# Performance work log

Measured on AMD Instinct MI355X. Metric: run time of the kernel, lower is better.

## Reference

```python
import jax, jax.numpy as jnp
import numpy as np

STEPS = 8

def wn_linear(x, v, g, b):
    # PyTorch weight_norm (dim=0): w = g * v / ||v||_row
    w = v * (g / jnp.linalg.norm(v, axis=1, keepdims=True))
    return x @ w.T + b

def setup_inputs() -> dict:
    key = jax.random.key(0)
    ks = jax.random.split(key, 24)
    N, L, H = 65536, 256, 512
    D = L + 3
    inp = {
        'input': jax.random.normal(ks[0], (N, D), jnp.float32),
        # LSTMCell params
        'W_ih': jax.random.normal(ks[1], (4 * H, D), jnp.float32) * (1.0 / np.sqrt(D)),
        'b_ih': jnp.zeros((4 * H,), jnp.float32),
        'W_hh': jax.random.normal(ks[2], (4 * H, H), jnp.float32) * (1.0 / np.sqrt(H)),
        'b_hh': jnp.zeros((4 * H,), jnp.float32).at[H:2 * H].set(1.0),  # forget-gate init
        # affine out layer (initialized tiny in the original)
        'W_aff': jax.random.normal(ks[3], (6, H), jnp.float32) * 1e-3,
        'b_aff': jnp.zeros((6,), jnp.float32),
    }
    # SdfDecoder: lin0..lin4 weight-normed, lin5 plain
    dims_in = [3, 256, 256, 256, 256]
    for i, din in enumerate(dims_in):
        inp[f'v{i}'] = jax.random.normal(ks[4 + 2 * i], (256, din), jnp.float32) * (1.0 / np.sqrt(din))
        inp[f'g{i}'] = jnp.linalg.norm(inp[f'v{i}'], axis=1, keepdims=True)
        inp[f'b{i}'] = jnp.zeros((256,), jnp.float32)
    inp['W5'] = jax.random.normal(ks[20], (1, 256), jnp.float32) * (1.0 / 16.0)
    inp['b5'] = jnp.zeros((1,), jnp.float32)
    return inp

def warp(code, xyz0, W_ih, b_ih, W_hh, b_hh, W_aff, b_aff):
    N = code.shape[0]
    H = W_hh.shape[1]
    def step(carry, _):
        h, c, xyz = carry
        x = jnp.concatenate([code, xyz], axis=1)               # [N, L+3]
        gates = x @ W_ih.T + b_ih + h @ W_hh.T + b_hh          # [N, 4H]
        i, f, g, o = jnp.split(gates, 4, axis=1)
        c = jax.nn.sigmoid(f) * c + jax.nn.sigmoid(i) * jnp.tanh(g)
        h = o_ = jax.nn.sigmoid(o) * jnp.tanh(c)
        a = h @ W_aff.T + b_aff                                # [N, 6]
        xyz = a[:, 3:] + (1.0 + a[:, :3]) * xyz                # addcmul
        return (h, c, xyz), None
    z = jnp.zeros((N, H), code.dtype)
    (_, _, xyz), _ = jax.lax.scan(step, (z, z, xyz0), None, length=STEPS)
    return xyz

def sdf_decoder(p, v0, g0, b0, v1, g1, b1, v2, g2, b2, v3, g3, b3, v4, g4, b4, W5, b5):
    x = jax.nn.relu(wn_linear(p, v0, g0, b0))   # eval mode: dropout is identity
    x = jax.nn.relu(wn_linear(x, v1, g1, b1))
    x = jax.nn.relu(wn_linear(x, v2, g2, b2))
    x = jax.nn.relu(wn_linear(x, v3, g3, b3))
    x = jax.nn.relu(wn_linear(x, v4, g4, b4))
    return x @ W5.T + b5

def reference(input, W_ih, b_ih, W_hh, b_hh, W_aff, b_aff,
              v0, g0, b0, v1, g1, b1, v2, g2, b2, v3, g3, b3, v4, g4, b4, W5, b5):
    code, xyz = input[:, :-3], input[:, -3:]
    p_final = warp(code, xyz, W_ih, b_ih, W_hh, b_hh, W_aff, b_aff)
    return sdf_decoder(p_final, v0, g0, b0, v1, g1, b1, v2, g2, b2, v3, g3, b3, v4, g4, b4, W5, b5)
```

## Files before the change

kernel.cpp:

```cpp
#include <hip/hip_runtime.h>
#include <stdint.h>


typedef short v8s __attribute__((ext_vector_type(8)));
typedef float v4f __attribute__((ext_vector_type(4)));

#define MFMA16(a, b, c) __builtin_amdgcn_mfma_f32_16x16x32_bf16((a), (b), (c), 0, 0, 0)

static __device__ __forceinline__ unsigned short f2bf(float f) {
  union { float f; uint32_t u; } x; x.f = f;
  uint32_t u = x.u;
  return (unsigned short)((u + 0x7fffu + ((u >> 16) & 1u)) >> 16);
}
static __device__ __forceinline__ float bf2f(unsigned short s) {
  union { uint32_t u; float f; } x; x.u = ((uint32_t)s) << 16; return x.f;
}
static __device__ __forceinline__ float sigf(float x) {
  return 1.f / (1.f + __expf(-x));
}
static __device__ __forceinline__ float tanh_fast(float x) {
  float e = __expf(2.f * x);
  return 1.f - 2.f / (e + 1.f);
}

static __device__ __forceinline__ void gload16(const void* g, void* l) {
  __builtin_amdgcn_global_load_lds(
      (const __attribute__((address_space(1))) uint32_t*)g,
      (__attribute__((address_space(3))) uint32_t*)l, 16, 0, 0);
}

#define WS_LSTMPK 0
#define WS_LSTMPK_ELEMS 1638400
#define WS_AFFPK 3276800
#define WS_AFFPK_ELEMS 8192
#define WS_DECPK 3293184
#define WS_DECPK_ELEMS 262144
#define WS_DSCALE 3817472
#define WS_TOTAL 3821568

#define OFF_H     0
#define OFF_RING  65536
#define OFF_AFF   114688
#define OFF_BIASP 131072
#define OFF_XYZ   139264
#define OFF_A     140288
#define OFF_W0N   142336
#define OFF_B0    145408
#define OFF_DB    146432
#define OFF_W5    150528
#define OFF_MISC  151552
#define SMEM_BYTES 151616

__global__ void dec_norm_kernel(const float* __restrict__ v1, const float* __restrict__ v2,
                                const float* __restrict__ v3, const float* __restrict__ v4,
                                const float* __restrict__ g1, const float* __restrict__ g2,
                                const float* __restrict__ g3, const float* __restrict__ g4,
                                float* __restrict__ dscale) {
  int L = blockIdx.x;
  int row = threadIdx.x;
  const float* v = (L == 0) ? v1 : (L == 1) ? v2 : (L == 2) ? v3 : v4;
  const float* g = (L == 0) ? g1 : (L == 1) ? g2 : (L == 2) ? g3 : g4;
  float s = 0.f;
  for (int k = 0; k < 256; ++k) { float x = v[row * 256 + k]; s += x * x; }
  dscale[L * 256 + row] = g[row] / sqrtf(s);
}

__global__ void pack_kernel(const float* __restrict__ W_ih, const float* __restrict__ W_hh,
                            const float* __restrict__ W_aff,
                            const float* __restrict__ v1, const float* __restrict__ v2,
                            const float* __restrict__ v3, const float* __restrict__ v4,
                            const float* __restrict__ dscale,
                            unsigned short* __restrict__ lstmpk,
                            unsigned short* __restrict__ affpk,
                            unsigned short* __restrict__ decpk) {
  int i = blockIdx.x * 256 + threadIdx.x;
  if (i < WS_LSTMPK_ELEMS) {
    int j = i & 7; int rest = i >> 3;
    int l = rest & 63; rest >>= 6;
    int fi = rest & 15; rest >>= 4;
    int tb = rest % 25; int c = rest / 25;
    int kl = 8 * (l >> 4) + j;
    int grow = (fi & 3) * 512 + c * 64 + (fi >> 2) * 16 + (l & 15);
    float val;
    if (tb < 8)       val = W_ih[(size_t)grow * 259 + tb * 32 + kl];
    else if (tb == 8) val = (kl < 3) ? W_ih[(size_t)grow * 259 + 256 + kl] : 0.f;
    else              val = W_hh[(size_t)grow * 512 + (tb - 9) * 32 + kl];
    lstmpk[i] = f2bf(val);
  } else if (i < WS_LSTMPK_ELEMS + WS_AFFPK_ELEMS) {
    int ii = i - WS_LSTMPK_ELEMS;
    int j = ii & 7, l = (ii >> 3) & 63, t = ii >> 9;
    int k = 32 * t + 8 * (l >> 4) + j;
    int col = l & 15;
    float val = (col < 6) ? W_aff[col * 512 + k] : 0.f;
    affpk[ii] = f2bf(val);
  } else {
    int ii = i - (WS_LSTMPK_ELEMS + WS_AFFPK_ELEMS);
    int j = ii & 7, l = (ii >> 3) & 63, fi = (ii >> 9) & 15, t = (ii >> 13) & 7, L = ii >> 16;
    int k = 32 * t + 8 * (l >> 4) + j;
    int col = 16 * fi + (l & 15);
    const float* v = (L == 0) ? v1 : (L == 1) ? v2 : (L == 2) ? v3 : v4;
    float val = v[col * 256 + k] * dscale[L * 256 + col];
    decpk[ii] = f2bf(val);
  }
}

__global__ __launch_bounds__(512, 1) void lstm_main(
    const float* __restrict__ input,
    const float* __restrict__ b_ih, const float* __restrict__ b_hh,
    const float* __restrict__ b_aff,
    const float* __restrict__ v0, const float* __restrict__ g0, const float* __restrict__ b0,
    const float* __restrict__ b1, const float* __restrict__ b2,
    const float* __restrict__ b3, const float* __restrict__ b4,
    const float* __restrict__ W5, const float* __restrict__ b5,
    const unsigned short* __restrict__ lstmpk,
    const unsigned short* __restrict__ affpk,
    const unsigned short* __restrict__ decpk,
    float* __restrict__ out) {
  extern __shared__ char smem[];
  float* smf = (float*)smem;

  const int tid = threadIdx.x;
  const int lane = tid & 63;
  const int wid = tid >> 6;
  const int l15 = lane & 15;
  const int lg = lane >> 4;
  const int rowg = wid & 1;
  const int colq = wid >> 1;
  const int r0 = blockIdx.x * 64;

  const int arow0 = rowg * 32 + l15;
  const int arow1 = arow0 + 16;
  const uint32_t a_sw = (uint32_t)((l15 & 7) << 4);
  const uint32_t hbase0 = OFF_H + (uint32_t)arow0 * 1024;
  const uint32_t hbase1 = OFF_H + (uint32_t)arow1 * 1024;
  const char* lstm_c = (const char*)lstmpk;
  const char* dec_c = (const char*)decpk;

  {
    uint4 z = make_uint4(0, 0, 0, 0);
    for (int i = tid; i < 4096; i += 512) *(uint4*)(smem + OFF_H + (size_t)i * 16) = z;
  }
  if (tid < 192) {
    int row = tid / 3, d = tid - row * 3;
    smf[OFF_XYZ / 4 + row * 4 + d] = input[(size_t)(r0 + row) * 259 + 256 + d];
  }
  for (int i = tid; i < 2048; i += 512) {
    int c = i >> 8, jc = i & 255, n = jc >> 4, t15 = jc & 15;
    int grow = (n & 3) * 512 + c * 64 + (n >> 2) * 16 + t15;
    smf[OFF_BIASP / 4 + i] = b_ih[grow] + b_hh[grow];
  }
  if (tid < 256) {
    int u = tid;
    float a0 = v0[u * 3 + 0], a1 = v0[u * 3 + 1], a2 = v0[u * 3 + 2];
    float sc = g0[u] / sqrtf(a0 * a0 + a1 * a1 + a2 * a2);
    smf[OFF_W0N / 4 + u * 3 + 0] = a0 * sc;
    smf[OFF_W0N / 4 + u * 3 + 1] = a1 * sc;
    smf[OFF_W0N / 4 + u * 3 + 2] = a2 * sc;
    smf[OFF_B0 / 4 + u] = b0[u];
    smf[OFF_DB / 4 + 0 * 256 + u] = b1[u];
    smf[OFF_DB / 4 + 1 * 256 + u] = b2[u];
    smf[OFF_DB / 4 + 2 * 256 + u] = b3[u];
    smf[OFF_DB / 4 + 3 * 256 + u] = b4[u];
    smf[OFF_W5 / 4 + u] = W5[u];
  }
  if (tid < 6) smf[OFF_MISC / 4 + tid] = b_aff[tid];
  if (tid == 6) smf[OFF_MISC / 4 + 6] = b5[0];
  {
    const char* src = (const char*)affpk + (((size_t)(2 * wid)) << 10) + (size_t)lane * 16;
    char* dst = smem + OFF_AFF + ((2 * wid) << 10);
    gload16(src, dst);
    gload16(src + 1024, dst + 1024);
  }

  v8s codeA0[8], codeA1[8];
  {
    const float* cr0 = input + (size_t)(r0 + arow0) * 259;
    const float* cr1 = input + (size_t)(r0 + arow1) * 259;
#pragma unroll
    for (int t = 0; t < 8; ++t) {
      v8s a0v = {0, 0, 0, 0, 0, 0, 0, 0}, a1v = {0, 0, 0, 0, 0, 0, 0, 0};
#pragma unroll
      for (int j = 0; j < 8; ++j) {
        a0v[j] = (short)f2bf(cr0[t * 32 + lg * 8 + j]);
        a1v[j] = (short)f2bf(cr1[t * 32 + lg * 8 + j]);
      }
      codeA0[t] = a0v; codeA1[t] = a1v;
    }
  }
  __syncthreads();

  float creg[8][8];
#pragma unroll
  for (int c = 0; c < 8; ++c)
#pragma unroll
    for (int e = 0; e < 8; ++e) creg[c][e] = 0.f;
  uint32_t hst[8][4];

  for (int step = 0; step < 8; ++step) {
    v8s xyzA0 = {0, 0, 0, 0, 0, 0, 0, 0}, xyzA1 = {0, 0, 0, 0, 0, 0, 0, 0};
    if (lg == 0) {
      xyzA0[0] = (short)f2bf(smf[OFF_XYZ / 4 + arow0 * 4 + 0]);
      xyzA0[1] = (short)f2bf(smf[OFF_XYZ / 4 + arow0 * 4 + 1]);
      xyzA0[2] = (short)f2bf(smf[OFF_XYZ / 4 + arow0 * 4 + 2]);
      xyzA1[0] = (short)f2bf(smf[OFF_XYZ / 4 + arow1 * 4 + 0]);
      xyzA1[1] = (short)f2bf(smf[OFF_XYZ / 4 + arow1 * 4 + 1]);
      xyzA1[2] = (short)f2bf(smf[OFF_XYZ / 4 + arow1 * 4 + 2]);
    }

    int cs = 0, tbs = 0, rs = 2, sb = 0;
    {
      const char* s0 = lstm_c + (((size_t)(2 * wid)) << 10) + (size_t)lane * 16;
      char* d0 = smem + OFF_RING + ((2 * wid) << 10);
      gload16(s0, d0); gload16(s0 + 1024, d0 + 1024);
      const char* s1 = lstm_c + (((size_t)(16 + 2 * wid)) << 10) + (size_t)lane * 16;
      char* d1 = smem + OFF_RING + 16384 + ((2 * wid) << 10);
      gload16(s1, d1); gload16(s1 + 1024, d1 + 1024);
      tbs = 2;
    }

#pragma unroll
    for (int c = 0; c < 8; ++c) {
      v4f acc0[4], acc1[4];
#pragma unroll
      for (int fi = 0; fi < 4; ++fi) {
        float bb = smf[OFF_BIASP / 4 + c * 256 + (colq * 4 + fi) * 16 + l15];
        acc0[fi][0] = bb; acc0[fi][1] = bb; acc0[fi][2] = bb; acc0[fi][3] = bb;
        acc1[fi][0] = bb; acc1[fi][1] = bb; acc1[fi][2] = bb; acc1[fi][3] = bb;
      }

      auto phase = [&](v8s af0, v8s af1, bool last) {
        if (last) { asm volatile("s_waitcnt vmcnt(0)" ::: "memory"); }
        else      { asm volatile("s_waitcnt vmcnt(2)" ::: "memory"); }
        __builtin_amdgcn_s_barrier();
        if (cs < 8) {
          const char* src = lstm_c + (((size_t)((cs * 25 + tbs) * 16 + 2 * wid)) << 10)
                          + (size_t)lane * 16;
          char* dst = smem + OFF_RING + rs * 16384 + ((2 * wid) << 10);
          gload16(src, dst);
          gload16(src + 1024, dst + 1024);
          rs = (rs == 2) ? 0 : rs + 1;
          if (++tbs == 25) { tbs = 0; ++cs; }
        }
        const char* sl = smem + OFF_RING + sb * 16384 + (colq << 12) + (lane << 4);
        __builtin_amdgcn_s_setprio(1);
#pragma unroll
        for (int fi = 0; fi < 4; ++fi) {
          v8s bf = *(const v8s*)(sl + (fi << 10));
          acc0[fi] = MFMA16(af0, bf, acc0[fi]);
          acc1[fi] = MFMA16(af1, bf, acc1[fi]);
        }
        __builtin_amdgcn_s_setprio(0);
        sb = (sb == 2) ? 0 : sb + 1;
      };

#pragma unroll
      for (int t = 0; t < 8; ++t) phase(codeA0[t], codeA1[t], false);
      phase(xyzA0, xyzA1, false);
#pragma unroll 2
      for (int t2 = 0; t2 < 16; ++t2) {
        uint32_t ko = (uint32_t)(t2 * 32 + lg * 8) * 2;
        v8s af0 = *(const v8s*)(smem + hbase0 + (ko ^ a_sw));
        v8s af1 = *(const v8s*)(smem + hbase1 + (ko ^ a_sw));
        phase(af0, af1, (c == 7) && (t2 == 15));
      }

#define CELLUP(AQ, M) do {                                                   \
        uint32_t plo = 0, phi = 0;                                           \
        _Pragma("unroll")                                                    \
        for (int j = 0; j < 4; ++j) {                                        \
          float gi = AQ[0][j], gf = AQ[1][j], gg = AQ[2][j], go = AQ[3][j];  \
          float cc = creg[c][(M) * 4 + j];                                   \
          cc = sigf(gf) * cc + sigf(gi) * tanh_fast(gg);                     \
          creg[c][(M) * 4 + j] = cc;                                         \
          uint32_t hb = f2bf(sigf(go) * tanh_fast(cc));                      \
          if (j < 2) plo |= hb << (16 * j); else phi |= hb << (16 * (j - 2));\
        }                                                                    \
        hst[c][(M) * 2 + 0] = plo; hst[c][(M) * 2 + 1] = phi; } while (0)
      CELLUP(acc0, 0);
      CELLUP(acc1, 1);
#undef CELLUP
    }

    __syncthreads();
#pragma unroll
    for (int c = 0; c < 8; ++c)
#pragma unroll
      for (int m = 0; m < 2; ++m)
#pragma unroll
        for (int j = 0; j < 4; ++j) {
          int u = c * 64 + colq * 16 + l15;
          int rr = rowg * 32 + m * 16 + lg * 4 + j;
          uint32_t val = ((j < 2) ? (hst[c][m * 2] >> (16 * j))
                                  : (hst[c][m * 2 + 1] >> (16 * (j - 2)))) & 0xffffu;
          *(unsigned short*)(smem + OFF_H + (uint32_t)rr * 1024 +
                             (uint32_t)((u * 2) ^ ((rr & 7) << 4))) = (unsigned short)val;
        }
    __syncthreads();
    if (wid < 2) {
      v4f a0 = {0.f, 0.f, 0.f, 0.f}, a1v = {0.f, 0.f, 0.f, 0.f};
#pragma unroll 2
      for (int t = 0; t < 16; ++t) {
        uint32_t ko = (uint32_t)(t * 32 + lg * 8) * 2;
        v8s bf = *(const v8s*)(smem + OFF_AFF + (t << 10) + (lane << 4));
        v8s af0 = *(const v8s*)(smem + hbase0 + (ko ^ a_sw));
        v8s af1 = *(const v8s*)(smem + hbase1 + (ko ^ a_sw));
        a0 = MFMA16(af0, bf, a0);
        a1v = MFMA16(af1, bf, a1v);
      }
      if (l15 < 6) {
        float ba = smf[OFF_MISC / 4 + l15];
#pragma unroll
        for (int j = 0; j < 4; ++j) {
          smf[OFF_A / 4 + (rowg * 32 + lg * 4 + j) * 8 + l15] = a0[j] + ba;
          smf[OFF_A / 4 + (rowg * 32 + 16 + lg * 4 + j) * 8 + l15] = a1v[j] + ba;
        }
      }
    }
    __syncthreads();
    if (tid < 192) {
      int rr = tid / 3, d = tid - rr * 3;
      float ad = smf[OFF_A / 4 + rr * 8 + d];
      float a3 = smf[OFF_A / 4 + rr * 8 + 3 + d];
      float old = smf[OFF_XYZ / 4 + rr * 4 + d];
      smf[OFF_XYZ / 4 + rr * 4 + d] = a3 + (1.f + ad) * old;
    }
    __syncthreads();
  }

  {
    const char* s0 = dec_c + (((size_t)(2 * wid)) << 10) + (size_t)lane * 16;
    char* d0 = smem + OFF_RING + ((2 * wid) << 10);
    gload16(s0, d0); gload16(s0 + 1024, d0 + 1024);
    const char* s1 = dec_c + (((size_t)(16 + 2 * wid)) << 10) + (size_t)lane * 16;
    char* d1 = smem + OFF_RING + 16384 + ((2 * wid) << 10);
    gload16(s1, d1); gload16(s1 + 1024, d1 + 1024);
  }
  {
    int row = tid & 63;
    int ublk = tid >> 6;
    float p0 = smf[OFF_XYZ / 4 + row * 4 + 0];
    float p1 = smf[OFF_XYZ / 4 + row * 4 + 1];
    float p2 = smf[OFF_XYZ / 4 + row * 4 + 2];
#pragma unroll
    for (int gq = 0; gq < 4; ++gq) {
      int u0 = ublk * 32 + gq * 8;
      uint32_t pk[4];
#pragma unroll
      for (int jj = 0; jj < 8; ++jj) {
        int uu = u0 + jj;
        float val = smf[OFF_B0 / 4 + uu]
                  + smf[OFF_W0N / 4 + uu * 3 + 0] * p0
                  + smf[OFF_W0N / 4 + uu * 3 + 1] * p1
                  + smf[OFF_W0N / 4 + uu * 3 + 2] * p2;
        val = fmaxf(val, 0.f);
        ((unsigned short*)pk)[jj] = f2bf(val);
      }
      *(uint4*)(smem + OFF_H + (uint32_t)row * 512 +
                (uint32_t)((u0 * 2) ^ ((row & 7) << 4))) = *(uint4*)pk;
    }
  }
  __syncthreads();

  {
    int ps = 2, rs = 2, sb = 0;
#pragma unroll
    for (int L = 0; L < 4; ++L) {
      v4f acc0[4], acc1[4];
#pragma unroll
      for (int fi = 0; fi < 4; ++fi) {
        float bb = smf[OFF_DB / 4 + L * 256 + (colq * 4 + fi) * 16 + l15];
        acc0[fi][0] = bb; acc0[fi][1] = bb; acc0[fi][2] = bb; acc0[fi][3] = bb;
        acc1[fi][0] = bb; acc1[fi][1] = bb; acc1[fi][2] = bb; acc1[fi][3] = bb;
      }
      uint32_t xin = OFF_H + (uint32_t)((L & 1) * 32768);
      uint32_t ab0 = xin + (uint32_t)arow0 * 512;
      uint32_t ab1 = xin + (uint32_t)arow1 * 512;
#pragma unroll
      for (int t = 0; t < 8; ++t) {
        uint32_t ko = (uint32_t)(t * 32 + lg * 8) * 2;
        v8s af0 = *(const v8s*)(smem + ab0 + (ko ^ a_sw));
        v8s af1 = *(const v8s*)(smem + ab1 + (ko ^ a_sw));
        if (L == 3 && t == 7) { asm volatile("s_waitcnt vmcnt(0)" ::: "memory"); }
        else                  { asm volatile("s_waitcnt vmcnt(2)" ::: "memory"); }
        __builtin_amdgcn_s_barrier();
        if (ps < 32) {
          const char* src = dec_c + (((size_t)(ps * 16 + 2 * wid)) << 10) + (size_t)lane * 16;
          char* dst = smem + OFF_RING + rs * 16384 + ((2 * wid) << 10);
          gload16(src, dst);
          gload16(src + 1024, dst + 1024);
          ps++;
          rs = (rs == 2) ? 0 : rs + 1;
        }
        const char* sl = smem + OFF_RING + sb * 16384 + (colq << 12) + (lane << 4);
        __builtin_amdgcn_s_setprio(1);
#pragma unroll
        for (int fi = 0; fi < 4; ++fi) {
          v8s bf = *(const v8s*)(sl + (fi << 10));
          acc0[fi] = MFMA16(af0, bf, acc0[fi]);
          acc1[fi] = MFMA16(af1, bf, acc1[fi]);
        }
        __builtin_amdgcn_s_setprio(0);
        sb = (sb == 2) ? 0 : sb + 1;
      }
      uint32_t xout = OFF_H + (uint32_t)(((L + 1) & 1) * 32768);
#pragma unroll
      for (int fi = 0; fi < 4; ++fi) {
        int coli = (colq * 4 + fi) * 16 + l15;
#pragma unroll
        for (int j = 0; j < 4; ++j) {
          int rr0 = rowg * 32 + lg * 4 + j;
          int rr1 = rr0 + 16;
          *(unsigned short*)(smem + xout + (uint32_t)rr0 * 512 +
                             (uint32_t)((coli * 2) ^ ((rr0 & 7) << 4))) = f2bf(fmaxf(acc0[fi][j], 0.f));
          *(unsigned short*)(smem + xout + (uint32_t)rr1 * 512 +
                             (uint32_t)((coli * 2) ^ ((rr1 & 7) << 4))) = f2bf(fmaxf(acc1[fi][j], 0.f));
        }
      }
      __syncthreads();
    }
  }

  {
    float b5v = smf[OFF_MISC / 4 + 6];
    for (int rr = 0; rr < 8; ++rr) {
      int r = wid * 8 + rr;
      uint32_t byteoff = OFF_H + (uint32_t)r * 512 + (uint32_t)((lane * 8) ^ ((r & 7) << 4));
      uint2 xv = *(const uint2*)(smem + byteoff);
      float p = 0.f;
#pragma unroll
      for (int jj = 0; jj < 4; ++jj) {
        unsigned short us = (unsigned short)(((jj < 2) ? (xv.x >> (16 * jj))
                                                       : (xv.y >> (16 * (jj - 2)))) & 0xffffu);
        p += bf2f(us) * smf[OFF_W5 / 4 + lane * 4 + jj];
      }
#pragma unroll
      for (int off = 32; off >= 1; off >>= 1) p += __shfl_xor(p, off, 64);
      if (lane == 0) out[r0 + r] = p + b5v;
    }
  }
}

extern "C" void kernel_launch(void* const* d_in, const int* in_sizes, int n_in,
                              void* d_out, int out_size, void* d_ws, size_t ws_size,
                              hipStream_t stream) {
  const float* input = (const float*)d_in[0];
  const float* W_ih  = (const float*)d_in[1];
  const float* b_ih  = (const float*)d_in[2];
  const float* W_hh  = (const float*)d_in[3];
  const float* b_hh  = (const float*)d_in[4];
  const float* W_aff = (const float*)d_in[5];
  const float* b_aff = (const float*)d_in[6];
  const float* v0 = (const float*)d_in[7];
  const float* g0 = (const float*)d_in[8];
  const float* b0 = (const float*)d_in[9];
  const float* v1 = (const float*)d_in[10];
  const float* g1 = (const float*)d_in[11];
  const float* b1 = (const float*)d_in[12];
  const float* v2 = (const float*)d_in[13];
  const float* g2 = (const float*)d_in[14];
  const float* b2 = (const float*)d_in[15];
  const float* v3 = (const float*)d_in[16];
  const float* g3 = (const float*)d_in[17];
  const float* b3 = (const float*)d_in[18];
  const float* v4 = (const float*)d_in[19];
  const float* g4 = (const float*)d_in[20];
  const float* b4 = (const float*)d_in[21];
  const float* W5 = (const float*)d_in[22];
  const float* b5 = (const float*)d_in[23];

  char* ws = (char*)d_ws;
  unsigned short* lstmpk = (unsigned short*)(ws + WS_LSTMPK);
  unsigned short* affpk  = (unsigned short*)(ws + WS_AFFPK);
  unsigned short* decpk  = (unsigned short*)(ws + WS_DECPK);
  float* dscale = (float*)(ws + WS_DSCALE);
  float* outp = (float*)d_out;

  (void)in_sizes; (void)n_in; (void)out_size; (void)ws_size;

  hipFuncSetAttribute((const void*)lstm_main,
                      hipFuncAttributeMaxDynamicSharedMemorySize, SMEM_BYTES);

  dec_norm_kernel<<<4, 256, 0, stream>>>(v1, v2, v3, v4, g1, g2, g3, g4, dscale);
  pack_kernel<<<7456, 256, 0, stream>>>(W_ih, W_hh, W_aff, v1, v2, v3, v4, dscale,
                                        lstmpk, affpk, decpk);
  lstm_main<<<1024, 512, SMEM_BYTES, stream>>>(
      input, b_ih, b_hh, b_aff, v0, g0, b0, b1, b2, b3, b4, W5, b5,
      lstmpk, affpk, decpk, outp);
}
```

Baseline: 4.223 ms.

## Skip zero-state recurrent GEMM, stage code in LDS, rotate weight chunk order

At step 0 the recurrent h·W_hh phases are skipped, because h starts at zero. The bf16 code operand moves from per-thread registers into a swizzled LDS buffer, which frees VGPRs. The affine weights now stream through the shared ring buffer as a final slab, and the next step's first slabs are prefetched during the xyz update. Each block also rotates which gate chunk it starts on, to spread L2 traffic, and several biases and the first-layer weights are stored as bf16 in LDS. That last change loses a little precision.

```diff
diff --git a/kernel.cpp b/kernel.cpp
--- a/kernel.cpp
+++ b/kernel.cpp
@@ -40,16 +40,16 @@
 
 #define OFF_H     0
 #define OFF_RING  65536
-#define OFF_AFF   114688
-#define OFF_BIASP 131072
-#define OFF_XYZ   139264
-#define OFF_A     140288
-#define OFF_W0N   142336
-#define OFF_B0    145408
-#define OFF_DB    146432
-#define OFF_W5    150528
-#define OFF_MISC  151552
-#define SMEM_BYTES 151616
+#define OFF_CODE  114688
+#define OFF_BIASP 147456
+#define OFF_XYZ   151552
+#define OFF_A     152576
+#define OFF_W0N   154624
+#define OFF_B0    156160
+#define OFF_DB    157184
+#define OFF_W5    159232
+#define OFF_MISC  160256
+#define SMEM_BYTES 160288
 
 __global__ void dec_norm_kernel(const float* __restrict__ v1, const float* __restrict__ v2,
                                 const float* __restrict__ v3, const float* __restrict__ v4,
@@ -118,6 +118,7 @@
     float* __restrict__ out) {
   extern __shared__ char smem[];
   float* smf = (float*)smem;
+  uint16_t* smh = (uint16_t*)smem;
 
   const int tid = threadIdx.x;
   const int lane = tid & 63;
@@ -127,18 +128,44 @@
   const int rowg = wid & 1;
   const int colq = wid >> 1;
   const int r0 = blockIdx.x * 64;
+  const int rot = blockIdx.x & 7;
 
   const int arow0 = rowg * 32 + l15;
   const int arow1 = arow0 + 16;
   const uint32_t a_sw = (uint32_t)((l15 & 7) << 4);
   const uint32_t hbase0 = OFF_H + (uint32_t)arow0 * 1024;
   const uint32_t hbase1 = OFF_H + (uint32_t)arow1 * 1024;
+  const uint32_t cbase0 = OFF_CODE + (uint32_t)arow0 * 512;
+  const uint32_t cbase1 = OFF_CODE + (uint32_t)arow1 * 512;
   const char* lstm_c = (const char*)lstmpk;
+  const char* aff_c = (const char*)affpk;
   const char* dec_c = (const char*)decpk;
 
+  auto stage_slab = [&](const char* slab_base, int slot) {
+    const char* src = slab_base + ((2 * wid) << 10) + (size_t)lane * 16;
+    char* dst = smem + OFF_RING + slot * 16384 + ((2 * wid) << 10);
+    gload16(src, dst);
+    gload16(src + 1024, dst + 1024);
+  };
+
   {
-    uint4 z = make_uint4(0, 0, 0, 0);
-    for (int i = tid; i < 4096; i += 512) *(uint4*)(smem + OFF_H + (size_t)i * 16) = z;
+    int row = tid >> 3;
+    int kb0 = (tid & 7) * 8;
+    const float* src0 = input + (size_t)(r0 + row) * 259;
+#pragma unroll
+    for (int it = 0; it < 4; ++it) {
+      int kb = kb0 + it * 64;
+      const float* src = src0 + kb;
+      uint32_t p[4];
+#pragma unroll
+      for (int jj = 0; jj < 4; ++jj) {
+        float f0 = src[2 * jj], f1 = src[2 * jj + 1];
+        p[jj] = (uint32_t)f2bf(f0) | ((uint32_t)f2bf(f1) << 16);
+      }
+      uint32_t byteoff = OFF_CODE + (uint32_t)row * 512 +
+                         (uint32_t)((kb * 2) ^ ((row & 7) << 4));
+      *(uint4*)(smem + byteoff) = make_uint4(p[0], p[1], p[2], p[3]);
+    }
   }
   if (tid < 192) {
     int row = tid / 3, d = tid - row * 3;
@@ -147,47 +174,28 @@
   for (int i = tid; i < 2048; i += 512) {
     int c = i >> 8, jc = i & 255, n = jc >> 4, t15 = jc & 15;
     int grow = (n & 3) * 512 + c * 64 + (n >> 2) * 16 + t15;
-    smf[OFF_BIASP / 4 + i] = b_ih[grow] + b_hh[grow];
+    smh[OFF_BIASP / 2 + i] = f2bf(b_ih[grow] + b_hh[grow]);
   }
   if (tid < 256) {
     int u = tid;
     float a0 = v0[u * 3 + 0], a1 = v0[u * 3 + 1], a2 = v0[u * 3 + 2];
     float sc = g0[u] / sqrtf(a0 * a0 + a1 * a1 + a2 * a2);
-    smf[OFF_W0N / 4 + u * 3 + 0] = a0 * sc;
-    smf[OFF_W0N / 4 + u * 3 + 1] = a1 * sc;
-    smf[OFF_W0N / 4 + u * 3 + 2] = a2 * sc;
+    smh[OFF_W0N / 2 + u * 3 + 0] = f2bf(a0 * sc);
+    smh[OFF_W0N / 2 + u * 3 + 1] = f2bf(a1 * sc);
+    smh[OFF_W0N / 2 + u * 3 + 2] = f2bf(a2 * sc);
     smf[OFF_B0 / 4 + u] = b0[u];
-    smf[OFF_DB / 4 + 0 * 256 + u] = b1[u];
-    smf[OFF_DB / 4 + 1 * 256 + u] = b2[u];
-    smf[OFF_DB / 4 + 2 * 256 + u] = b3[u];
-    smf[OFF_DB / 4 + 3 * 256 + u] = b4[u];
+    smh[OFF_DB / 2 + 0 * 256 + u] = f2bf(b1[u]);
+    smh[OFF_DB / 2 + 1 * 256 + u] = f2bf(b2[u]);
+    smh[OFF_DB / 2 + 2 * 256 + u] = f2bf(b3[u]);
+    smh[OFF_DB / 2 + 3 * 256 + u] = f2bf(b4[u]);
     smf[OFF_W5 / 4 + u] = W5[u];
   }
   if (tid < 6) smf[OFF_MISC / 4 + tid] = b_aff[tid];
   if (tid == 6) smf[OFF_MISC / 4 + 6] = b5[0];
-  {
-    const char* src = (const char*)affpk + (((size_t)(2 * wid)) << 10) + (size_t)lane * 16;
-    char* dst = smem + OFF_AFF + ((2 * wid) << 10);
-    gload16(src, dst);
-    gload16(src + 1024, dst + 1024);
-  }
-
-  v8s codeA0[8], codeA1[8];
-  {
-    const float* cr0 = input + (size_t)(r0 + arow0) * 259;
-    const float* cr1 = input + (size_t)(r0 + arow1) * 259;
-#pragma unroll
-    for (int t = 0; t < 8; ++t) {
-      v8s a0v = {0, 0, 0, 0, 0, 0, 0, 0}, a1v = {0, 0, 0, 0, 0, 0, 0, 0};
-#pragma unroll
-      for (int j = 0; j < 8; ++j) {
-        a0v[j] = (short)f2bf(cr0[t * 32 + lg * 8 + j]);
-        a1v[j] = (short)f2bf(cr1[t * 32 + lg * 8 + j]);
-      }
-      codeA0[t] = a0v; codeA1[t] = a1v;
-    }
-  }
   __syncthreads();
+
+  stage_slab(lstm_c + ((size_t)(rot * 25) << 14), 0);
+  stage_slab(lstm_c + ((size_t)(rot * 25 + 1) << 14), 1);
 
   float creg[8][8];
 #pragma unroll
@@ -197,6 +205,9 @@
   uint32_t hst[8][4];
 
   for (int step = 0; step < 8; ++step) {
+    const int per_c = step ? 25 : 9;
+    const int count = per_c * 8 + 1;
+
     v8s xyzA0 = {0, 0, 0, 0, 0, 0, 0, 0}, xyzA1 = {0, 0, 0, 0, 0, 0, 0, 0};
     if (lg == 0) {
       xyzA0[0] = (short)f2bf(smf[OFF_XYZ / 4 + arow0 * 4 + 0]);
@@ -207,116 +218,129 @@
       xyzA1[2] = (short)f2bf(smf[OFF_XYZ / 4 + arow1 * 4 + 2]);
     }
 
-    int cs = 0, tbs = 0, rs = 2, sb = 0;
-    {
-      const char* s0 = lstm_c + (((size_t)(2 * wid)) << 10) + (size_t)lane * 16;
-      char* d0 = smem + OFF_RING + ((2 * wid) << 10);
-      gload16(s0, d0); gload16(s0 + 1024, d0 + 1024);
-      const char* s1 = lstm_c + (((size_t)(16 + 2 * wid)) << 10) + (size_t)lane * 16;
-      char* d1 = smem + OFF_RING + 16384 + ((2 * wid) << 10);
-      gload16(s1, d1); gload16(s1 + 1024, d1 + 1024);
-      tbs = 2;
-    }
-
-#pragma unroll
-    for (int c = 0; c < 8; ++c) {
-      v4f acc0[4], acc1[4];
+    int sS = 2, stbs = 2, scs_phys = rot, rs = 2, sb = 0;
+
+    v4f acc0[4], acc1[4];
+    auto phz = [&](v8s af0, v8s af1) {
+      asm volatile("s_waitcnt vmcnt(2)" ::: "memory");
+      __builtin_amdgcn_s_barrier();
+      if (sS < count) {
+        const char* src;
+        if (sS == count - 1) {
+          src = aff_c + ((2 * wid) << 10) + (size_t)lane * 16;
+        } else {
+          src = lstm_c + (((size_t)((scs_phys * 25 + stbs) * 16 + 2 * wid)) << 10)
+              + (size_t)lane * 16;
+          if (++stbs == per_c) { stbs = 0; scs_phys = (scs_phys + 1) & 7; }
+        }
+        char* dst = smem + OFF_RING + rs * 16384 + ((2 * wid) << 10);
+        gload16(src, dst);
+        gload16(src + 1024, dst + 1024);
+        ++sS;
+        rs = (rs == 2) ? 0 : rs + 1;
+      }
+      const char* sl = smem + OFF_RING + sb * 16384 + (colq << 12) + (lane << 4);
+      __builtin_amdgcn_s_setprio(1);
 #pragma unroll
       for (int fi = 0; fi < 4; ++fi) {
-        float bb = smf[OFF_BIASP / 4 + c * 256 + (colq * 4 + fi) * 16 + l15];
+        v8s bf = *(const v8s*)(sl + (fi << 10));
+        acc0[fi] = MFMA16(af0, bf, acc0[fi]);
+        acc1[fi] = MFMA16(af1, bf, acc1[fi]);
+      }
+      __builtin_amdgcn_s_setprio(0);
+      sb = (sb == 2) ? 0 : sb + 1;
+    };
+
+#pragma unroll
+    for (int ci = 0; ci < 8; ++ci) {
+      const int cphys = (ci + rot) & 7;
+#pragma unroll
+      for (int fi = 0; fi < 4; ++fi) {
+        float bb = bf2f(smh[OFF_BIASP / 2 + cphys * 256 + (colq * 4 + fi) * 16 + l15]);
         acc0[fi][0] = bb; acc0[fi][1] = bb; acc0[fi][2] = bb; acc0[fi][3] = bb;
         acc1[fi][0] = bb; acc1[fi][1] = bb; acc1[fi][2] = bb; acc1[fi][3] = bb;
       }
-
-      auto phase = [&](v8s af0, v8s af1, bool last) {
-        if (last) { asm volatile("s_waitcnt vmcnt(0)" ::: "memory"); }
-        else      { asm volatile("s_waitcnt vmcnt(2)" ::: "memory"); }
-        __builtin_amdgcn_s_barrier();
-        if (cs < 8) {
-          const char* src = lstm_c + (((size_t)((cs * 25 + tbs) * 16 + 2 * wid)) << 10)
-                          + (size_t)lane * 16;
-          char* dst = smem + OFF_RING + rs * 16384 + ((2 * wid) << 10);
-          gload16(src, dst);
-          gload16(src + 1024, dst + 1024);
-          rs = (rs == 2) ? 0 : rs + 1;
-          if (++tbs == 25) { tbs = 0; ++cs; }
-        }
-        const char* sl = smem + OFF_RING + sb * 16384 + (colq << 12) + (lane << 4);
-        __builtin_amdgcn_s_setprio(1);
-#pragma unroll
-        for (int fi = 0; fi < 4; ++fi) {
-          v8s bf = *(const v8s*)(sl + (fi << 10));
-          acc0[fi] = MFMA16(af0, bf, acc0[fi]);
-          acc1[fi] = MFMA16(af1, bf, acc1[fi]);
-        }
-        __builtin_amdgcn_s_setprio(0);
-        sb = (sb == 2) ? 0 : sb + 1;
-      };
-
-#pragma unroll
-      for (int t = 0; t < 8; ++t) phase(codeA0[t], codeA1[t], false);
-      phase(xyzA0, xyzA1, false);
 #pragma unroll 2
-      for (int t2 = 0; t2 < 16; ++t2) {
-        uint32_t ko = (uint32_t)(t2 * 32 + lg * 8) * 2;
-        v8s af0 = *(const v8s*)(smem + hbase0 + (ko ^ a_sw));
-        v8s af1 = *(const v8s*)(smem + hbase1 + (ko ^ a_sw));
-        phase(af0, af1, (c == 7) && (t2 == 15));
-      }
-
+      for (int t = 0; t < 8; ++t) {
+        uint32_t ko = (uint32_t)(t * 64 + lg * 16);
+        v8s af0 = *(const v8s*)(smem + cbase0 + (ko ^ a_sw));
+        v8s af1 = *(const v8s*)(smem + cbase1 + (ko ^ a_sw));
+        phz(af0, af1);
+      }
+      phz(xyzA0, xyzA1);
+      if (step > 0) {
+#pragma unroll 2
+        for (int t2 = 0; t2 < 16; ++t2) {
+          uint32_t ko = (uint32_t)(t2 * 64 + lg * 16);
+          v8s af0 = *(const v8s*)(smem + hbase0 + (ko ^ a_sw));
+          v8s af1 = *(const v8s*)(smem + hbase1 + (ko ^ a_sw));
+          phz(af0, af1);
+        }
+      }
 #define CELLUP(AQ, M) do {                                                   \
         uint32_t plo = 0, phi = 0;                                           \
         _Pragma("unroll")                                                    \
         for (int j = 0; j < 4; ++j) {                                        \
           float gi = AQ[0][j], gf = AQ[1][j], gg = AQ[2][j], go = AQ[3][j];  \
-          float cc = creg[c][(M) * 4 + j];                                   \
+          float cc = creg[ci][(M) * 4 + j];                                  \
           cc = sigf(gf) * cc + sigf(gi) * tanh_fast(gg);                     \
-          creg[c][(M) * 4 + j] = cc;                                         \
+          creg[ci][(M) * 4 + j] = cc;                                        \
           uint32_t hb = f2bf(sigf(go) * tanh_fast(cc));                      \
           if (j < 2) plo |= hb << (16 * j); else phi |= hb << (16 * (j - 2));\
         }                                                                    \
-        hst[c][(M) * 2 + 0] = plo; hst[c][(M) * 2 + 1] = phi; } while (0)
+        hst[ci][(M) * 2 + 0] = plo; hst[ci][(M) * 2 + 1] = phi; } while (0)
       CELLUP(acc0, 0);
       CELLUP(acc1, 1);
 #undef CELLUP
     }
 
+    asm volatile("s_waitcnt vmcnt(0)" ::: "memory");
     __syncthreads();
 #pragma unroll
-    for (int c = 0; c < 8; ++c)
+    for (int ci = 0; ci < 8; ++ci) {
+      const int cphys = (ci + rot) & 7;
 #pragma unroll
       for (int m = 0; m < 2; ++m)
 #pragma unroll
         for (int j = 0; j < 4; ++j) {
-          int u = c * 64 + colq * 16 + l15;
+          int u = cphys * 64 + colq * 16 + l15;
           int rr = rowg * 32 + m * 16 + lg * 4 + j;
-          uint32_t val = ((j < 2) ? (hst[c][m * 2] >> (16 * j))
-                                  : (hst[c][m * 2 + 1] >> (16 * (j - 2)))) & 0xffffu;
+          uint32_t val = ((j < 2) ? (hst[ci][m * 2] >> (16 * j))
+                                  : (hst[ci][m * 2 + 1] >> (16 * (j - 2)))) & 0xffffu;
           *(unsigned short*)(smem + OFF_H + (uint32_t)rr * 1024 +
                              (uint32_t)((u * 2) ^ ((rr & 7) << 4))) = (unsigned short)val;
         }
+    }
     __syncthreads();
-    if (wid < 2) {
-      v4f a0 = {0.f, 0.f, 0.f, 0.f}, a1v = {0.f, 0.f, 0.f, 0.f};
+    {
+      const uint32_t affslot = (uint32_t)(((count - 1) % 3) * 16384);
+      if (wid < 2) {
+        v4f a0 = {0.f, 0.f, 0.f, 0.f}, a1v = {0.f, 0.f, 0.f, 0.f};
 #pragma unroll 2
-      for (int t = 0; t < 16; ++t) {
-        uint32_t ko = (uint32_t)(t * 32 + lg * 8) * 2;
-        v8s bf = *(const v8s*)(smem + OFF_AFF + (t << 10) + (lane << 4));
-        v8s af0 = *(const v8s*)(smem + hbase0 + (ko ^ a_sw));
-        v8s af1 = *(const v8s*)(smem + hbase1 + (ko ^ a_sw));
-        a0 = MFMA16(af0, bf, a0);
-        a1v = MFMA16(af1, bf, a1v);
-      }
-      if (l15 < 6) {
-        float ba = smf[OFF_MISC / 4 + l15];
-#pragma unroll
-        for (int j = 0; j < 4; ++j) {
-          smf[OFF_A / 4 + (rowg * 32 + lg * 4 + j) * 8 + l15] = a0[j] + ba;
-          smf[OFF_A / 4 + (rowg * 32 + 16 + lg * 4 + j) * 8 + l15] = a1v[j] + ba;
+        for (int t = 0; t < 16; ++t) {
+          uint32_t ko = (uint32_t)(t * 64 + lg * 16);
+          v8s bf = *(const v8s*)(smem + OFF_RING + affslot + (t << 10) + (lane << 4));
+          v8s af0 = *(const v8s*)(smem + hbase0 + (ko ^ a_sw));
+          v8s af1 = *(const v8s*)(smem + hbase1 + (ko ^ a_sw));
+          a0 = MFMA16(af0, bf, a0);
+          a1v = MFMA16(af1, bf, a1v);
+        }
+        if (l15 < 6) {
+          float ba = smf[OFF_MISC / 4 + l15];
+#pragma unroll
+          for (int j = 0; j < 4; ++j) {
+            smf[OFF_A / 4 + (rowg * 32 + lg * 4 + j) * 8 + l15] = a0[j] + ba;
+            smf[OFF_A / 4 + (rowg * 32 + 16 + lg * 4 + j) * 8 + l15] = a1v[j] + ba;
+          }
         }
       }
     }
     __syncthreads();
+    {
+      const char* nsrc = (step == 7) ? dec_c : (lstm_c + ((size_t)(rot * 25) << 14));
+      stage_slab(nsrc, 0);
+      stage_slab(nsrc + 16384, 1);
+    }
     if (tid < 192) {
       int rr = tid / 3, d = tid - rr * 3;
       float ad = smf[OFF_A / 4 + rr * 8 + d];
@@ -328,14 +352,6 @@
   }
 
   {
-    const char* s0 = dec_c + (((size_t)(2 * wid)) << 10) + (size_t)lane * 16;
-    char* d0 = smem + OFF_RING + ((2 * wid) << 10);
-    gload16(s0, d0); gload16(s0 + 1024, d0 + 1024);
-    const char* s1 = dec_c + (((size_t)(16 + 2 * wid)) << 10) + (size_t)lane * 16;
-    char* d1 = smem + OFF_RING + 16384 + ((2 * wid) << 10);
-    gload16(s1, d1); gload16(s1 + 1024, d1 + 1024);
-  }
-  {
     int row = tid & 63;
     int ublk = tid >> 6;
     float p0 = smf[OFF_XYZ / 4 + row * 4 + 0];
@@ -349,9 +365,9 @@
       for (int jj = 0; jj < 8; ++jj) {
         int uu = u0 + jj;
         float val = smf[OFF_B0 / 4 + uu]
-                  + smf[OFF_W0N / 4 + uu * 3 + 0] * p0
-                  + smf[OFF_W0N / 4 + uu * 3 + 1] * p1
-                  + smf[OFF_W0N / 4 + uu * 3 + 2] * p2;
+                  + bf2f(smh[OFF_W0N / 2 + uu * 3 + 0]) * p0
+                  + bf2f(smh[OFF_W0N / 2 + uu * 3 + 1]) * p1
+                  + bf2f(smh[OFF_W0N / 2 + uu * 3 + 2]) * p2;
         val = fmaxf(val, 0.f);
         ((unsigned short*)pk)[jj] = f2bf(val);
       }
@@ -368,7 +384,7 @@
       v4f acc0[4], acc1[4];
 #pragma unroll
       for (int fi = 0; fi < 4; ++fi) {
-        float bb = smf[OFF_DB / 4 + L * 256 + (colq * 4 + fi) * 16 + l15];
+        float bb = bf2f(smh[OFF_DB / 2 + L * 256 + (colq * 4 + fi) * 16 + l15]);
         acc0[fi][0] = bb; acc0[fi][1] = bb; acc0[fi][2] = bb; acc0[fi][3] = bb;
         acc1[fi][0] = bb; acc1[fi][1] = bb; acc1[fi][2] = bb; acc1[fi][3] = bb;
       }
@@ -377,7 +393,7 @@
       uint32_t ab1 = xin + (uint32_t)arow1 * 512;
 #pragma unroll
       for (int t = 0; t < 8; ++t) {
-        uint32_t ko = (uint32_t)(t * 32 + lg * 8) * 2;
+        uint32_t ko = (uint32_t)(t * 64 + lg * 16);
         v8s af0 = *(const v8s*)(smem + ab0 + (ko ^ a_sw));
         v8s af1 = *(const v8s*)(smem + ab1 + (ko ^ a_sw));
         if (L == 3 && t == 7) { asm volatile("s_waitcnt vmcnt(0)" ::: "memory"); }
```

Measured after the change: 3.614 ms. -14.4%, faster.
